# Performance work log

Hardware: AMD Instinct MI355X
Metric: run time of the kernel (lower is better)

## Reference

```python
import jax, jax.numpy as jnp
import numpy as np
from jax import lax

B, N, C = 32, 2048, 256
S, NSAMP, RADIUS = 128, 16, 0.3
NH, NS, NC = 12, 10, 10
OUT_DIM = 5 + 2 * NH + 4 * NS + NC  # 79
EPS = 1e-5
MEAN_SIZES = np.array([[0.76584, 1.398258, 0.472728], [2.114256, 1.6203, 0.927272], [0.404671, 1.071108, 1.688889], [0.591958, 0.552978, 0.827272], [0.69519, 1.346299, 0.736364], [0.528526, 1.002642, 1.172878], [0.500618, 0.632163, 0.683424], [0.923508, 1.867419, 0.845495], [0.791118, 1.279516, 0.718182], [0.699104, 0.454178, 0.75625]], dtype=np.float32)


def _bn(x, g, be, m, v):
    # eval-mode batchnorm over trailing channel dim
    return (x - m) * (g / jnp.sqrt(v + EPS)) + be


def _fps(xyz, npoint):
    # farthest point sampling, sequential over npoint via scan, vectorized over batch
    Bb, Nn, _ = xyz.shape
    def step(carry, _):
        mind, last = carry  # [B,N], [B]
        lp = jnp.take_along_axis(xyz, last[:, None, None], axis=1)  # [B,1,3]
        d = jnp.sum((xyz - lp) ** 2, axis=-1)
        mind = jnp.minimum(mind, d)
        nxt = jnp.argmax(mind, axis=-1).astype(jnp.int32)
        return (mind, nxt), last
    init = (jnp.full((Bb, Nn), 1e10, xyz.dtype), jnp.zeros((Bb,), jnp.int32))
    _, inds = lax.scan(step, init, None, length=npoint)
    return jnp.transpose(inds)  # [B, npoint]


def _ball_query(xyz, new_xyz, radius, nsample):
    # first-nsample points within radius of each center (pad with first hit)
    Nn = xyz.shape[1]
    d2 = jnp.sum((new_xyz[:, :, None, :] - xyz[:, None, :, :]) ** 2, axis=-1)  # [B,S,N]
    cand = jnp.where(d2 < radius * radius, jnp.arange(Nn, dtype=jnp.int32)[None, None, :], Nn)
    idx = jnp.sort(cand, axis=-1)[..., :nsample]
    first = idx[..., :1]  # center itself is always within radius (d=0)
    return jnp.where(idx == Nn, first, idx)


def _forward(xyz, features, w0, bb0, g0, be0, m0, v0, w1, bb1, g1, be1, m1, v1, w2, bb2, g2, be2, m2, v2, c1w, c1b, g3, be3, m3, v3, c2w, c2b, g4, be4, m4, v4, c3w, c3b):
    fps_idx = _fps(xyz, S)  # [B,S]
    new_xyz = jnp.take_along_axis(xyz, fps_idx[..., None], axis=1)  # [B,S,3]
    idx = _ball_query(xyz, new_xyz, RADIUS, NSAMP)  # [B,S,ns]
    bidx = jnp.arange(xyz.shape[0])[:, None, None]
    g_xyz = (xyz[bidx, idx] - new_xyz[:, :, None, :]) / RADIUS  # normalize_xyz
    g_feat = jnp.transpose(features, (0, 2, 1))[bidx, idx]  # [B,S,ns,C]
    x = jnp.concatenate([g_xyz, g_feat], axis=-1)  # [B,S,ns,C+3]
    for w, bb, g, be, m, v in ((w0, bb0, g0, be0, m0, v0), (w1, bb1, g1, be1, m1, v1), (w2, bb2, g2, be2, m2, v2)):
        x = jax.nn.relu(_bn(x @ w + bb, g, be, m, v))
    x = jnp.max(x, axis=2)  # [B,S,128] pooled features
    net = jax.nn.relu(_bn(x @ c1w + c1b, g3, be3, m3, v3))
    net = jax.nn.relu(_bn(net @ c2w + c2b, g4, be4, m4, v4))
    net = net @ c3w + c3b  # [B,S,79] == torch net.transpose(2,1)
    obj = net[..., 0:2]
    ctr = new_xyz + net[..., 2:5]
    hs = net[..., 5:5 + NH]
    hrn = net[..., 5 + NH:5 + 2 * NH]
    hr = hrn * jnp.float32(np.pi / NH)
    ss = net[..., 5 + 2 * NH:5 + 2 * NH + NS]
    srn = net[..., 5 + 2 * NH + NS:5 + 2 * NH + 4 * NS].reshape(net.shape[0], S, NS, 3)
    sr = srn * jnp.asarray(MEAN_SIZES)[None, None]
    sem = net[..., 5 + 2 * NH + 4 * NS:]
    return jnp.concatenate([new_xyz, obj, ctr, hs, hrn, hr, ss, srn.reshape(net.shape[0], S, NS * 3), sr.reshape(net.shape[0], S, NS * 3), sem], axis=-1)  # [B,S,124]


def setup_inputs() -> dict:
    key = jax.random.key(0)
    ks = jax.random.split(key, 40)
    def w(k, shp):
        return jax.random.normal(k, shp, jnp.float32) * 0.05
    d = {"xyz": jax.random.normal(ks[0], (B, N, 3), jnp.float32), "features": jax.random.normal(ks[1], (B, C, N), jnp.float32)}
    i = 2
    for li, (cin, cout) in enumerate(((C + 3, 128), (128, 128), (128, 128))):
        d[f"w{li}"] = w(ks[i], (cin, cout)); d[f"bb{li}"] = w(ks[i + 1], (cout,))
        d[f"g{li}"] = 1.0 + w(ks[i + 2], (cout,)); d[f"be{li}"] = w(ks[i + 3], (cout,))
        d[f"m{li}"] = w(ks[i + 4], (cout,)); d[f"v{li}"] = jnp.ones((cout,), jnp.float32)
        i += 5
    d["c1w"] = w(ks[i], (128, 128)); d["c1b"] = w(ks[i + 1], (128,))
    d["g3"] = 1.0 + w(ks[i + 2], (128,)); d["be3"] = w(ks[i + 3], (128,)); d["m3"] = w(ks[i + 4], (128,)); d["v3"] = jnp.ones((128,), jnp.float32)
    d["c2w"] = w(ks[i + 5], (128, 128)); d["c2b"] = w(ks[i + 6], (128,))
    d["g4"] = 1.0 + w(ks[i + 7], (128,)); d["be4"] = w(ks[i + 8], (128,)); d["m4"] = w(ks[i + 9], (128,)); d["v4"] = jnp.ones((128,), jnp.float32)
    d["c3w"] = w(ks[i + 10], (128, OUT_DIM)); d["c3b"] = w(ks[i + 11], (OUT_DIM,))
    return d


def reference(xyz, features, w0, bb0, g0, be0, m0, v0, w1, bb1, g1, be1, m1, v1, w2, bb2, g2, be2, m2, v2, c1w, c1b, g3, be3, m3, v3, c2w, c2b, g4, be4, m4, v4, c3w, c3b):
    return _forward(xyz, features, w0, bb0, g0, be0, m0, v0, w1, bb1, g1, be1, m1, v1, w2, bb2, g2, be2, m2, v2, c1w, c1b, g3, be3, m3, v3, c2w, c2b, g4, be4, m4, v4, c3w, c3b)
```

## Files before the change

### kernel.cpp

```cpp
#include <hip/hip_runtime.h>
#include <hip/hip_bf16.h>
#include <math.h>

#define Bn 32
#define Nn 2048
#define Cc 256
#define Sn 128
#define KK 16
#define H 128
#define OUTC 79
#define ODIM 124
#define KP1 288

typedef __attribute__((ext_vector_type(8))) short short8;
typedef __attribute__((ext_vector_type(4))) float f32x4;
typedef unsigned long long ull;

__device__ __constant__ float MEANF[30] = {
    0.76584f, 1.398258f, 0.472728f,
    2.114256f, 1.6203f, 0.927272f,
    0.404671f, 1.071108f, 1.688889f,
    0.591958f, 0.552978f, 0.827272f,
    0.69519f, 1.346299f, 0.736364f,
    0.528526f, 1.002642f, 1.172878f,
    0.500618f, 0.632163f, 0.683424f,
    0.923508f, 1.867419f, 0.845495f,
    0.791118f, 1.279516f, 0.718182f,
    0.699104f, 0.454178f, 0.75625f};

__device__ __forceinline__ unsigned short f2bf(float f) {
    __hip_bfloat16 h = __float2bfloat16(f);
    return *reinterpret_cast<unsigned short*>(&h);
}

__device__ __forceinline__ ull umax64(ull a, ull b) { return a > b ? a : b; }

struct SmemFPS {
    float xs[Nn * 3];
    ull red[2][4];
    float nx[Sn * 3];
};
struct SmemT {
    float tile[64][33];
};
__global__ __launch_bounds__(256) void fps_transpose_kernel(const float* __restrict__ xyz,
                                                            const float* __restrict__ features,
                                                            float* __restrict__ new_xyz,
                                                            unsigned short* __restrict__ fT) {
    __shared__ __align__(16) char smem_raw[sizeof(SmemT) > sizeof(SmemFPS) ? sizeof(SmemT)
                                                                           : sizeof(SmemFPS)];
    const int bid = blockIdx.x;
    if (bid >= Bn) {
        SmemT* sm = (SmemT*)smem_raw;
        const int tb = bid - Bn;
        const int b = tb >> 8;
        const int rem = tb & 255;
        const int n0 = (rem & 63) * 32;
        const int c0 = (rem >> 6) * 64;
        const int tx = threadIdx.x & 31;
        const int ty = threadIdx.x >> 5;
        for (int i = ty; i < 64; i += 8)
            sm->tile[i][tx] = features[((size_t)b * Cc + (c0 + i)) * Nn + n0 + tx];
        __syncthreads();
        for (int n = ty; n < 32; n += 8) {
            const float lo = sm->tile[tx * 2 + 0][n];
            const float hi = sm->tile[tx * 2 + 1][n];
            const unsigned int v = (unsigned int)f2bf(lo) | ((unsigned int)f2bf(hi) << 16);
            *reinterpret_cast<unsigned int*>(&fT[((size_t)b * Nn + (n0 + n)) * Cc + c0 + tx * 2]) = v;
        }
        return;
    }
    {
#pragma clang fp contract(off)
        SmemFPS* sm = (SmemFPS*)smem_raw;
        float* xs = sm->xs;
        const int b = bid;
        const int t = threadIdx.x;
        const int lane = t & 63;
        const int wv = t >> 6;

        {
            float4* xs4 = (float4*)xs;
            const float4* src = (const float4*)(xyz + (size_t)b * Nn * 3);
            for (int i = t; i < Nn * 3 / 4; i += 256) xs4[i] = src[i];
        }
        __syncthreads();

        const int base = wv * 512 + lane;
        float px[8], py[8], pz[8], mind[8];
        int klo[8];
#pragma unroll
        for (int j = 0; j < 8; j++) {
            const int p = base + j * 64;
            px[j] = xs[p * 3 + 0];
            py[j] = xs[p * 3 + 1];
            pz[j] = xs[p * 3 + 2];
            mind[j] = 1e10f;
            klo[j] = 2047 - p;
        }
        float lx = xs[0], ly = xs[1], lz = xs[2];

        for (int it = 0; it < Sn; ++it) {
            if (t == 0) {
                sm->nx[it * 3 + 0] = lx;
                sm->nx[it * 3 + 1] = ly;
                sm->nx[it * 3 + 2] = lz;
            }
            ull kk[8];
#pragma unroll
            for (int j = 0; j < 8; j++) {
                const float dx = px[j] - lx;
                const float dy = py[j] - ly;
                const float dz = pz[j] - lz;
                const float dx2 = dx * dx;
                const float dy2 = dy * dy;
                const float dz2 = dz * dz;
                const float s01 = dx2 + dy2;
                const float d = s01 + dz2;
                const float m = fminf(mind[j], d);
                mind[j] = m;
                kk[j] = ((ull)__float_as_uint(m) << 32) | (unsigned int)klo[j];
            }
            ull k0 = umax64(kk[0], kk[1]);
            ull k1 = umax64(kk[2], kk[3]);
            ull k2 = umax64(kk[4], kk[5]);
            ull k3 = umax64(kk[6], kk[7]);
            k0 = umax64(k0, k1);
            k2 = umax64(k2, k3);
            ull bk = umax64(k0, k2);
#pragma unroll
            for (int off = 1; off < 64; off <<= 1) {
                const ull o = __shfl_xor(bk, off);
                bk = umax64(bk, o);
            }
            if (lane == 0) sm->red[it & 1][wv] = bk;
            __syncthreads();
            ull r0 = sm->red[it & 1][0];
            ull r1 = sm->red[it & 1][1];
            ull r2 = sm->red[it & 1][2];
            ull r3 = sm->red[it & 1][3];
            bk = umax64(umax64(r0, r1), umax64(r2, r3));
            const int last = 2047 - (int)(bk & 0xffffffffull);
            lx = xs[last * 3 + 0];
            ly = xs[last * 3 + 1];
            lz = xs[last * 3 + 2];
        }
        __syncthreads();
        for (int i = t; i < Sn * 3; i += 256)
            new_xyz[(size_t)b * Sn * 3 + i] = sm->nx[i];
    }
}

__device__ __forceinline__ float w0val(const float* __restrict__ w0, int n, int k) {
    if (k < 256) return w0[(3 + k) * H + n];
    if (k < 259) return w0[(k - 256) * H + n];
    return 0.0f;
}

__global__ __launch_bounds__(256) void prep_kernel(
    const float* __restrict__ w0, const float* __restrict__ bb0,
    const float* __restrict__ g0, const float* __restrict__ be0,
    const float* __restrict__ m0, const float* __restrict__ v0,
    const float* __restrict__ w1, const float* __restrict__ bb1,
    const float* __restrict__ g1, const float* __restrict__ be1,
    const float* __restrict__ m1, const float* __restrict__ v1,
    const float* __restrict__ w2, const float* __restrict__ bb2,
    const float* __restrict__ g2, const float* __restrict__ be2,
    const float* __restrict__ m2, const float* __restrict__ v2,
    const float* __restrict__ c1w, const float* __restrict__ c1b,
    const float* __restrict__ g3, const float* __restrict__ be3,
    const float* __restrict__ m3, const float* __restrict__ v3,
    const float* __restrict__ c2w, const float* __restrict__ c2b,
    const float* __restrict__ g4, const float* __restrict__ be4,
    const float* __restrict__ m4, const float* __restrict__ v4,
    const float* __restrict__ c3w, const float* __restrict__ c3b,
    unsigned short* __restrict__ Wf0, unsigned short* __restrict__ Wf1,
    unsigned short* __restrict__ Wf2, unsigned short* __restrict__ Wfc1,
    unsigned short* __restrict__ Wfc2, unsigned short* __restrict__ Wfc3,
    float* __restrict__ scbi, float* __restrict__ scbiH) {
    const int idx = blockIdx.x * 256 + threadIdx.x;

    if (idx < 4608) {
        const int kc = idx / 512;
        const int rem = idx & 511;
        const int nt = rem >> 6;
        const int lane = rem & 63;
        const int n = nt * 16 + (lane & 15);
        const int kb = kc * 32 + (lane >> 4) * 8;
        union { unsigned short u[8]; uint4 q; } P;
#pragma unroll
        for (int j = 0; j < 8; j++) P.u[j] = f2bf(w0val(w0, n, kb + j));
        ((uint4*)Wf0)[idx] = P.q;
    }
    if (idx < 2048) {
        const int kc = idx >> 9;
        const int rem = idx & 511;
        const int nt = rem >> 6;
        const int lane = rem & 63;
        const int n = nt * 16 + (lane & 15);
        const int kb = kc * 32 + (lane >> 4) * 8;
        union { unsigned short u[8]; uint4 q; } P1, P2, P3, P4;
#pragma unroll
        for (int j = 0; j < 8; j++) {
            const int k = kb + j;
            P1.u[j] = f2bf(w1[k * H + n]);
            P2.u[j] = f2bf(w2[k * H + n]);
            P3.u[j] = f2bf(c1w[k * H + n]);
            P4.u[j] = f2bf(c2w[k * H + n]);
        }
        ((uint4*)Wf1)[idx] = P1.q;
        ((uint4*)Wf2)[idx] = P2.q;
        ((uint4*)Wfc1)[idx] = P3.q;
        ((uint4*)Wfc2)[idx] = P4.q;
    }
    if (idx < 1280) {
        const int kc = idx / 320;
        const int rem = idx % 320;
        const int nt = rem / 64;
        const int lane = rem % 64;
        const int n = nt * 16 + (lane & 15);
        const int kb = kc * 32 + (lane >> 4) * 8;
        union { unsigned short u[8]; uint4 q; } P;
#pragma unroll
        for (int j = 0; j < 8; j++)
            P.u[j] = (n < OUTC) ? f2bf(c3w[(kb + j) * OUTC + n]) : (unsigned short)0;
        ((uint4*)Wfc3)[idx] = P.q;
    }
    if (idx < 128) {
        const float sc1 = g0[idx] / sqrtf(v0[idx] + 1e-5f);
        scbi[0 * 128 + idx] = sc1;
        scbi[1 * 128 + idx] = (bb0[idx] - m0[idx]) * sc1 + be0[idx];
        const float sc2 = g1[idx] / sqrtf(v1[idx] + 1e-5f);
        scbi[2 * 128 + idx] = sc2;
        scbi[3 * 128 + idx] = (bb1[idx] - m1[idx]) * sc2 + be1[idx];
        const float sc3 = g2[idx] / sqrtf(v2[idx] + 1e-5f);
        scbi[4 * 128 + idx] = sc3;
        scbi[5 * 128 + idx] = (bb2[idx] - m2[idx]) * sc3 + be2[idx];
        const float sA = g3[idx] / sqrtf(v3[idx] + 1e-5f);
        scbiH[0 * 128 + idx] = sA;
        scbiH[1 * 128 + idx] = (c1b[idx] - m3[idx]) * sA + be3[idx];
        const float sB = g4[idx] / sqrtf(v4[idx] + 1e-5f);
        scbiH[2 * 128 + idx] = sB;
        scbiH[3 * 128 + idx] = (c2b[idx] - m4[idx]) * sB + be4[idx];
    }
    if (idx < 80) scbiH[512 + idx] = (idx < OUTC) ? c3b[idx] : 0.0f;
}

#define YSTR 136
__global__ __launch_bounds__(256) void groupmlp_mfma_kernel(
    const float* __restrict__ xyz, const unsigned short* __restrict__ featT,
    const float* __restrict__ new_xyz,
    const unsigned short* __restrict__ Wf0, const unsigned short* __restrict__ Wf1,
    const unsigned short* __restrict__ Wf2, const float* __restrict__ scbi,
    unsigned short* __restrict__ pooledb) {
    const int wv = threadIdx.x >> 6;
    const int lane = threadIdx.x & 63;
    const int bs = blockIdx.x * 4 + wv;
    const int b = bs >> 7;
    const int mrow = lane & 15;
    const int quad = lane >> 4;

    __shared__ unsigned short ylds_all[4][16 * YSTR];
    __shared__ int sbuf[4][16];
    unsigned short* ylds = &ylds_all[wv][0];

    const float cx = new_xyz[bs * 3 + 0];
    const float cy = new_xyz[bs * 3 + 1];
    const float cz = new_xyz[bs * 3 + 2];
    int basec = 0;
    {
#pragma clang fp contract(off)
        for (int c0 = 0; c0 < Nn && basec < KK; c0 += 64) {
            const int p = c0 + lane;
            const float dx = xyz[((size_t)b * Nn + p) * 3 + 0] - cx;
            const float dy = xyz[((size_t)b * Nn + p) * 3 + 1] - cy;
            const float dz = xyz[((size_t)b * Nn + p) * 3 + 2] - cz;
            const float dx2 = dx * dx;
            const float dy2 = dy * dy;
            const float dz2 = dz * dz;
            const float s01 = dx2 + dy2;
            const float d2 = s01 + dz2;
            const bool q = d2 < 0.09f;
            const ull mask = __ballot(q);
            const int prefix = __popcll(mask & ((1ull << lane) - 1ull));
            const int slot = basec + prefix;
            if (q && slot < KK) sbuf[wv][slot] = p;
            basec += __popcll(mask);
        }
    }
    const int cnt = basec < KK ? basec : KK;
    const int p = sbuf[wv][mrow < cnt ? mrow : 0];

    const short8* arow = reinterpret_cast<const short8*>(featT + ((size_t)(b * Nn + p)) * Cc);

    short8 a1x = {0, 0, 0, 0, 0, 0, 0, 0};
    {
        const float fx = xyz[((size_t)(b * Nn + p)) * 3 + 0];
        const float fy = xyz[((size_t)(b * Nn + p)) * 3 + 1];
        const float fz = xyz[((size_t)(b * Nn + p)) * 3 + 2];
        if (quad == 0) {
            a1x.s0 = (short)f2bf((fx - cx) / 0.3f);
            a1x.s1 = (short)f2bf((fy - cy) / 0.3f);
            a1x.s2 = (short)f2bf((fz - cz) / 0.3f);
        }
    }

    const short8* wf0 = reinterpret_cast<const short8*>(Wf0);
    const short8* wf1 = reinterpret_cast<const short8*>(Wf1);
    const short8* wf2 = reinterpret_cast<const short8*>(Wf2);
    const short8* yv = reinterpret_cast<const short8*>(ylds);

    f32x4 acc[8] = {};

    {
        short8 acur = arow[quad];
        short8 anxt;
        short8 bcur[8], bnxt[8];
#pragma unroll
        for (int nt = 0; nt < 8; nt++)
            bcur[nt] = wf0[nt * 64 + lane];
        for (int kc = 0; kc < 9; kc++) {
            if (kc < 8) {
                if (kc < 7) anxt = arow[(kc + 1) * 4 + quad];
                else anxt = a1x;
#pragma unroll
                for (int nt = 0; nt < 8; nt++)
                    bnxt[nt] = wf0[((kc + 1) * 8 + nt) * 64 + lane];
            }
#pragma unroll
            for (int nt = 0; nt < 8; nt++)
                acc[nt] = __builtin_amdgcn_mfma_f32_16x16x32_bf16(acur, bcur[nt], acc[nt], 0, 0, 0);
            acur = anxt;
#pragma unroll
            for (int nt = 0; nt < 8; nt++) bcur[nt] = bnxt[nt];
        }
    }
#pragma unroll
    for (int nt = 0; nt < 8; nt++) {
        const int n = nt * 16 + mrow;
        const float sc = scbi[0 * 128 + n];
        const float bi = scbi[1 * 128 + n];
#pragma unroll
        for (int r = 0; r < 4; r++) {
            const float z = fmaxf(acc[nt][r] * sc + bi, 0.0f);
            ylds[(quad * 4 + r) * YSTR + n] = f2bf(z);
        }
    }

#pragma unroll
    for (int nt = 0; nt < 8; nt++) acc[nt] = (f32x4){0.f, 0.f, 0.f, 0.f};
    {
        short8 acur = yv[mrow * (YSTR / 8) + quad];
        short8 anxt;
        short8 bcur[8], bnxt[8];
#pragma unroll
        for (int nt = 0; nt < 8; nt++)
            bcur[nt] = wf1[nt * 64 + lane];
        for (int kc = 0; kc < 4; kc++) {
            if (kc < 3) {
                anxt = yv[mrow * (YSTR / 8) + (kc + 1) * 4 + quad];
#pragma unroll
                for (int nt = 0; nt < 8; nt++)
                    bnxt[nt] = wf1[((kc + 1) * 8 + nt) * 64 + lane];
            }
#pragma unroll
            for (int nt = 0; nt < 8; nt++)
                acc[nt] = __builtin_amdgcn_mfma_f32_16x16x32_bf16(acur, bcur[nt], acc[nt], 0, 0, 0);
            acur = anxt;
#pragma unroll
            for (int nt = 0; nt < 8; nt++) bcur[nt] = bnxt[nt];
        }
    }
#pragma unroll
    for (int nt = 0; nt < 8; nt++) {
        const int n = nt * 16 + mrow;
        const float sc = scbi[2 * 128 + n];
        const float bi = scbi[3 * 128 + n];
#pragma unroll
        for (int r = 0; r < 4; r++) {
            const float z = fmaxf(acc[nt][r] * sc + bi, 0.0f);
            ylds[(quad * 4 + r) * YSTR + n] = f2bf(z);
        }
    }

#pragma unroll
    for (int nt = 0; nt < 8; nt++) acc[nt] = (f32x4){0.f, 0.f, 0.f, 0.f};
    {
        short8 acur = yv[mrow * (YSTR / 8) + quad];
        short8 anxt;
        short8 bcur[8], bnxt[8];
#pragma unroll
        for (int nt = 0; nt < 8; nt++)
            bcur[nt] = wf2[nt * 64 + lane];
        for (int kc = 0; kc < 4; kc++) {
            if (kc < 3) {
                anxt = yv[mrow * (YSTR / 8) + (kc + 1) * 4 + quad];
#pragma unroll
                for (int nt = 0; nt < 8; nt++)
                    bnxt[nt] = wf2[((kc + 1) * 8 + nt) * 64 + lane];
            }
#pragma unroll
            for (int nt = 0; nt < 8; nt++)
                acc[nt] = __builtin_amdgcn_mfma_f32_16x16x32_bf16(acur, bcur[nt], acc[nt], 0, 0, 0);
            acur = anxt;
#pragma unroll
            for (int nt = 0; nt < 8; nt++) bcur[nt] = bnxt[nt];
        }
    }
#pragma unroll
    for (int nt = 0; nt < 8; nt++) {
        const int n = nt * 16 + mrow;
        const float sc = scbi[4 * 128 + n];
        const float bi = scbi[5 * 128 + n];
        float vmax = 0.0f;
#pragma unroll
        for (int r = 0; r < 4; r++)
            vmax = fmaxf(vmax, acc[nt][r] * sc + bi);
        vmax = fmaxf(vmax, __shfl_xor(vmax, 16));
        vmax = fmaxf(vmax, __shfl_xor(vmax, 32));
        if (quad == 0) pooledb[(size_t)bs * H + n] = f2bf(vmax);
    }
}

__global__ __launch_bounds__(64) void head_mfma_kernel(
    const unsigned short* __restrict__ pooledb, const float* __restrict__ new_xyz,
    const unsigned short* __restrict__ Wfc1, const unsigned short* __restrict__ Wfc2,
    const unsigned short* __restrict__ Wfc3, const float* __restrict__ scbiH,
    float* __restrict__ out) {
    const int lane = threadIdx.x;
    const int row0 = blockIdx.x * 16;
    const int mrow = lane & 15;
    const int quad = lane >> 4;

    __shared__ unsigned short ylds[16 * YSTR];
    __shared__ float flds[16 * 84];

    const short8* ar = reinterpret_cast<const short8*>(pooledb + (size_t)(row0 + mrow) * H);
    const short8* w1h = reinterpret_cast<const short8*>(Wfc1);
    const short8* w2h = reinterpret_cast<const short8*>(Wfc2);
    const short8* w3h = reinterpret_cast<const short8*>(Wfc3);
    const short8* yv = reinterpret_cast<const short8*>(ylds);

    f32x4 acc[8] = {};
#pragma unroll
    for (int kc = 0; kc < 4; kc++) {
        const short8 a = ar[kc * 4 + quad];
#pragma unroll
        for (int nt = 0; nt < 8; nt++) {
            const short8 bf = w1h[(kc * 8 + nt) * 64 + lane];
            acc[nt] = __builtin_amdgcn_mfma_f32_16x16x32_bf16(a, bf, acc[nt], 0, 0, 0);
        }
    }
#pragma unroll
    for (int nt = 0; nt < 8; nt++) {
        const int n = nt * 16 + mrow;
        const float sc = scbiH[0 * 128 + n];
        const float bi = scbiH[1 * 128 + n];
#pragma unroll
        for (int r = 0; r < 4; r++) {
            const float z = fmaxf(acc[nt][r] * sc + bi, 0.0f);
            ylds[(quad * 4 + r) * YSTR + n] = f2bf(z);
        }
    }

#pragma unroll
    for (int nt = 0; nt < 8; nt++) acc[nt] = (f32x4){0.f, 0.f, 0.f, 0.f};
#pragma unroll
    for (int kc = 0; kc < 4; kc++) {
        const short8 a = yv[mrow * (YSTR / 8) + kc * 4 + quad];
#pragma unroll
        for (int nt = 0; nt < 8; nt++) {
            const short8 bf = w2h[(kc * 8 + nt) * 64 + lane];
            acc[nt] = __builtin_amdgcn_mfma_f32_16x16x32_bf16(a, bf, acc[nt], 0, 0, 0);
        }
    }
#pragma unroll
    for (int nt = 0; nt < 8; nt++) {
        const int n = nt * 16 + mrow;
        const float sc = scbiH[2 * 128 + n];
        const float bi = scbiH[3 * 128 + n];
#pragma unroll
        for (int r = 0; r < 4; r++) {
            const float z = fmaxf(acc[nt][r] * sc + bi, 0.0f);
            ylds[(quad * 4 + r) * YSTR + n] = f2bf(z);
        }
    }

    f32x4 acc3[5] = {};
#pragma unroll
    for (int kc = 0; kc < 4; kc++) {
        const short8 a = yv[mrow * (YSTR / 8) + kc * 4 + quad];
#pragma unroll
        for (int nt = 0; nt < 5; nt++) {
            const short8 bf = w3h[(kc * 5 + nt) * 64 + lane];
            acc3[nt] = __builtin_amdgcn_mfma_f32_16x16x32_bf16(a, bf, acc3[nt], 0, 0, 0);
        }
    }
#pragma unroll
    for (int nt = 0; nt < 5; nt++) {
        const int n = nt * 16 + mrow;
        const float bi = scbiH[512 + n];
#pragma unroll
        for (int r = 0; r < 4; r++)
            flds[(quad * 4 + r) * 84 + n] = acc3[nt][r] + bi;
    }

    for (int m = 0; m < 16; m++) {
        const int row = row0 + m;
        const float* net = &flds[m * 84];
        const float* nz = new_xyz + (size_t)row * 3;
#pragma unroll
        for (int jj = 0; jj < 2; jj++) {
            const int j = lane + jj * 64;
            if (j < ODIM) {
                float val;
                if (j < 3) val = nz[j];
                else if (j < 5) val = net[j - 3];
                else if (j < 8) val = nz[j - 5] + net[2 + (j - 5)];
                else if (j < 20) val = net[5 + (j - 8)];
                else if (j < 32) val = net[17 + (j - 20)];
                else if (j < 44) val = net[17 + (j - 32)] * (float)(3.14159265358979323846 / 12.0);
                else if (j < 54) val = net[29 + (j - 44)];
                else if (j < 84) val = net[39 + (j - 54)];
                else if (j < 114) val = net[39 + (j - 84)] * MEANF[j - 84];
                else val = net[69 + (j - 114)];
                out[(size_t)row * ODIM + j] = val;
            }
        }
    }
}

extern "C" void kernel_launch(void* const* d_in, const int* in_sizes, int n_in,
                              void* d_out, int out_size, void* d_ws, size_t ws_size,
                              hipStream_t stream) {
    (void)in_sizes; (void)n_in; (void)out_size; (void)ws_size;
    const float* xyz = (const float*)d_in[0];
    const float* features = (const float*)d_in[1];
    const float* w0 = (const float*)d_in[2];
    const float* bb0 = (const float*)d_in[3];
    const float* g0 = (const float*)d_in[4];
    const float* be0 = (const float*)d_in[5];
    const float* m0 = (const float*)d_in[6];
    const float* v0 = (const float*)d_in[7];
    const float* w1 = (const float*)d_in[8];
    const float* bb1 = (const float*)d_in[9];
    const float* g1 = (const float*)d_in[10];
    const float* be1 = (const float*)d_in[11];
    const float* m1 = (const float*)d_in[12];
    const float* v1 = (const float*)d_in[13];
    const float* w2 = (const float*)d_in[14];
    const float* bb2 = (const float*)d_in[15];
    const float* g2 = (const float*)d_in[16];
    const float* be2 = (const float*)d_in[17];
    const float* m2 = (const float*)d_in[18];
    const float* v2 = (const float*)d_in[19];
    const float* c1w = (const float*)d_in[20];
    const float* c1b = (const float*)d_in[21];
    const float* g3 = (const float*)d_in[22];
    const float* be3 = (const float*)d_in[23];
    const float* m3 = (const float*)d_in[24];
    const float* v3 = (const float*)d_in[25];
    const float* c2w = (const float*)d_in[26];
    const float* c2b = (const float*)d_in[27];
    const float* g4 = (const float*)d_in[28];
    const float* be4 = (const float*)d_in[29];
    const float* m4 = (const float*)d_in[30];
    const float* v4 = (const float*)d_in[31];
    const float* c3w = (const float*)d_in[32];
    const float* c3b = (const float*)d_in[33];
    float* out = (float*)d_out;

    char* ws = (char*)d_ws;
    float* nxyz = (float*)(ws + 0);
    float* scbi = (float*)(ws + 49152);
    float* scbiH = (float*)(ws + 52224);
    unsigned short* Wf0 = (unsigned short*)(ws + 54592);
    unsigned short* Wf1 = (unsigned short*)(ws + 128320);
    unsigned short* Wf2 = (unsigned short*)(ws + 161088);
    unsigned short* Wfc1 = (unsigned short*)(ws + 193856);
    unsigned short* Wfc2 = (unsigned short*)(ws + 226624);
    unsigned short* Wfc3 = (unsigned short*)(ws + 259392);
    unsigned short* pooledb = (unsigned short*)(ws + 279872);
    unsigned short* featT = (unsigned short*)(ws + 804160);

    hipLaunchKernelGGL(prep_kernel, dim3(18), dim3(256), 0, stream,
                       w0, bb0, g0, be0, m0, v0,
                       w1, bb1, g1, be1, m1, v1,
                       w2, bb2, g2, be2, m2, v2,
                       c1w, c1b, g3, be3, m3, v3,
                       c2w, c2b, g4, be4, m4, v4,
                       c3w, c3b,
                       Wf0, Wf1, Wf2, Wfc1, Wfc2, Wfc3, scbi, scbiH);
    hipLaunchKernelGGL(fps_transpose_kernel, dim3(Bn + Bn * 256), dim3(256), 0, stream,
                       xyz, features, nxyz, featT);
    hipLaunchKernelGGL(groupmlp_mfma_kernel, dim3(Bn * Sn / 4), dim3(256), 0, stream,
                       xyz, featT, nxyz, Wf0, Wf1, Wf2, scbi, pooledb);
    hipLaunchKernelGGL(head_mfma_kernel, dim3(Bn * Sn / 16), dim3(64), 0, stream,
                       pooledb, nxyz, Wfc1, Wfc2, Wfc3, scbiH, out);
}
```

Baseline: 302.8 us.

## Fuse prep into FPS/transpose kernel and carry coordinates through FPS argmax reduction

Merges the weight-prep kernel into the FPS/transpose launch as extra blocks, which removes one kernel launch. The FPS loop now carries the winning point's coordinates through the argmax reduction, so each iteration no longer has to look up the chosen point in a shared xyz copy. That shared copy is removed, which shrinks LDS use. The cross-lane reduction uses ds_swizzle and a final bpermute in place of 64-bit shfl_xor; each step moves five 32-bit values instead of one 64-bit key.

```diff
diff --git a/kernel.cpp b/kernel.cpp
--- a/kernel.cpp
+++ b/kernel.cpp
@@ -33,131 +33,34 @@
     return *reinterpret_cast<unsigned short*>(&h);
 }
 
-__device__ __forceinline__ ull umax64(ull a, ull b) { return a > b ? a : b; }
+__device__ __forceinline__ float w0val(const float* __restrict__ w0, int n, int k) {
+    if (k < 256) return w0[(3 + k) * H + n];
+    if (k < 259) return w0[(k - 256) * H + n];
+    return 0.0f;
+}
+
+#define BFLY_SWZ(PAT)                                                          \
+    {                                                                          \
+        const int ohi = __builtin_amdgcn_ds_swizzle(hi, PAT);                  \
+        const int olo = __builtin_amdgcn_ds_swizzle(lo, PAT);                  \
+        const int oxi = __builtin_amdgcn_ds_swizzle(xi, PAT);                  \
+        const int oyi = __builtin_amdgcn_ds_swizzle(yi, PAT);                  \
+        const int ozi = __builtin_amdgcn_ds_swizzle(zi, PAT);                  \
+        const ull ok = ((ull)(unsigned)ohi << 32) | (unsigned)olo;             \
+        const ull ck = ((ull)(unsigned)hi << 32) | (unsigned)lo;               \
+        if (ok > ck) { hi = ohi; lo = olo; xi = oxi; yi = oyi; zi = ozi; }     \
+    }
 
 struct SmemFPS {
-    float xs[Nn * 3];
-    ull red[2][4];
+    int red[2][4][8];
     float nx[Sn * 3];
 };
 struct SmemT {
     float tile[64][33];
 };
-__global__ __launch_bounds__(256) void fps_transpose_kernel(const float* __restrict__ xyz,
-                                                            const float* __restrict__ features,
-                                                            float* __restrict__ new_xyz,
-                                                            unsigned short* __restrict__ fT) {
-    __shared__ __align__(16) char smem_raw[sizeof(SmemT) > sizeof(SmemFPS) ? sizeof(SmemT)
-                                                                           : sizeof(SmemFPS)];
-    const int bid = blockIdx.x;
-    if (bid >= Bn) {
-        SmemT* sm = (SmemT*)smem_raw;
-        const int tb = bid - Bn;
-        const int b = tb >> 8;
-        const int rem = tb & 255;
-        const int n0 = (rem & 63) * 32;
-        const int c0 = (rem >> 6) * 64;
-        const int tx = threadIdx.x & 31;
-        const int ty = threadIdx.x >> 5;
-        for (int i = ty; i < 64; i += 8)
-            sm->tile[i][tx] = features[((size_t)b * Cc + (c0 + i)) * Nn + n0 + tx];
-        __syncthreads();
-        for (int n = ty; n < 32; n += 8) {
-            const float lo = sm->tile[tx * 2 + 0][n];
-            const float hi = sm->tile[tx * 2 + 1][n];
-            const unsigned int v = (unsigned int)f2bf(lo) | ((unsigned int)f2bf(hi) << 16);
-            *reinterpret_cast<unsigned int*>(&fT[((size_t)b * Nn + (n0 + n)) * Cc + c0 + tx * 2]) = v;
-        }
-        return;
-    }
-    {
-#pragma clang fp contract(off)
-        SmemFPS* sm = (SmemFPS*)smem_raw;
-        float* xs = sm->xs;
-        const int b = bid;
-        const int t = threadIdx.x;
-        const int lane = t & 63;
-        const int wv = t >> 6;
-
-        {
-            float4* xs4 = (float4*)xs;
-            const float4* src = (const float4*)(xyz + (size_t)b * Nn * 3);
-            for (int i = t; i < Nn * 3 / 4; i += 256) xs4[i] = src[i];
-        }
-        __syncthreads();
-
-        const int base = wv * 512 + lane;
-        float px[8], py[8], pz[8], mind[8];
-        int klo[8];
-#pragma unroll
-        for (int j = 0; j < 8; j++) {
-            const int p = base + j * 64;
-            px[j] = xs[p * 3 + 0];
-            py[j] = xs[p * 3 + 1];
-            pz[j] = xs[p * 3 + 2];
-            mind[j] = 1e10f;
-            klo[j] = 2047 - p;
-        }
-        float lx = xs[0], ly = xs[1], lz = xs[2];
-
-        for (int it = 0; it < Sn; ++it) {
-            if (t == 0) {
-                sm->nx[it * 3 + 0] = lx;
-                sm->nx[it * 3 + 1] = ly;
-                sm->nx[it * 3 + 2] = lz;
-            }
-            ull kk[8];
-#pragma unroll
-            for (int j = 0; j < 8; j++) {
-                const float dx = px[j] - lx;
-                const float dy = py[j] - ly;
-                const float dz = pz[j] - lz;
-                const float dx2 = dx * dx;
-                const float dy2 = dy * dy;
-                const float dz2 = dz * dz;
-                const float s01 = dx2 + dy2;
-                const float d = s01 + dz2;
-                const float m = fminf(mind[j], d);
-                mind[j] = m;
-                kk[j] = ((ull)__float_as_uint(m) << 32) | (unsigned int)klo[j];
-            }
-            ull k0 = umax64(kk[0], kk[1]);
-            ull k1 = umax64(kk[2], kk[3]);
-            ull k2 = umax64(kk[4], kk[5]);
-            ull k3 = umax64(kk[6], kk[7]);
-            k0 = umax64(k0, k1);
-            k2 = umax64(k2, k3);
-            ull bk = umax64(k0, k2);
-#pragma unroll
-            for (int off = 1; off < 64; off <<= 1) {
-                const ull o = __shfl_xor(bk, off);
-                bk = umax64(bk, o);
-            }
-            if (lane == 0) sm->red[it & 1][wv] = bk;
-            __syncthreads();
-            ull r0 = sm->red[it & 1][0];
-            ull r1 = sm->red[it & 1][1];
-            ull r2 = sm->red[it & 1][2];
-            ull r3 = sm->red[it & 1][3];
-            bk = umax64(umax64(r0, r1), umax64(r2, r3));
-            const int last = 2047 - (int)(bk & 0xffffffffull);
-            lx = xs[last * 3 + 0];
-            ly = xs[last * 3 + 1];
-            lz = xs[last * 3 + 2];
-        }
-        __syncthreads();
-        for (int i = t; i < Sn * 3; i += 256)
-            new_xyz[(size_t)b * Sn * 3 + i] = sm->nx[i];
-    }
-}
-
-__device__ __forceinline__ float w0val(const float* __restrict__ w0, int n, int k) {
-    if (k < 256) return w0[(3 + k) * H + n];
-    if (k < 259) return w0[(k - 256) * H + n];
-    return 0.0f;
-}
-
-__global__ __launch_bounds__(256) void prep_kernel(
+__global__ __launch_bounds__(256) void fused_front_kernel(
+    const float* __restrict__ xyz, const float* __restrict__ features,
+    float* __restrict__ new_xyz, unsigned short* __restrict__ fT,
     const float* __restrict__ w0, const float* __restrict__ bb0,
     const float* __restrict__ g0, const float* __restrict__ be0,
     const float* __restrict__ m0, const float* __restrict__ v0,
@@ -178,72 +81,196 @@
     unsigned short* __restrict__ Wf2, unsigned short* __restrict__ Wfc1,
     unsigned short* __restrict__ Wfc2, unsigned short* __restrict__ Wfc3,
     float* __restrict__ scbi, float* __restrict__ scbiH) {
-    const int idx = blockIdx.x * 256 + threadIdx.x;
-
-    if (idx < 4608) {
-        const int kc = idx / 512;
-        const int rem = idx & 511;
-        const int nt = rem >> 6;
-        const int lane = rem & 63;
-        const int n = nt * 16 + (lane & 15);
-        const int kb = kc * 32 + (lane >> 4) * 8;
-        union { unsigned short u[8]; uint4 q; } P;
-#pragma unroll
-        for (int j = 0; j < 8; j++) P.u[j] = f2bf(w0val(w0, n, kb + j));
-        ((uint4*)Wf0)[idx] = P.q;
-    }
-    if (idx < 2048) {
-        const int kc = idx >> 9;
-        const int rem = idx & 511;
-        const int nt = rem >> 6;
-        const int lane = rem & 63;
-        const int n = nt * 16 + (lane & 15);
-        const int kb = kc * 32 + (lane >> 4) * 8;
-        union { unsigned short u[8]; uint4 q; } P1, P2, P3, P4;
+    __shared__ __align__(16) char smem_raw[sizeof(SmemT) > sizeof(SmemFPS) ? sizeof(SmemT)
+                                                                           : sizeof(SmemFPS)];
+    const int bid = blockIdx.x;
+    if (bid >= Bn + 8192) {
+        const int idx = (bid - (Bn + 8192)) * 256 + threadIdx.x;
+        if (idx < 4608) {
+            const int kc = idx / 512;
+            const int rem = idx & 511;
+            const int nt = rem >> 6;
+            const int lane = rem & 63;
+            const int n = nt * 16 + (lane & 15);
+            const int kb = kc * 32 + (lane >> 4) * 8;
+            union { unsigned short u[8]; uint4 q; } P;
+#pragma unroll
+            for (int j = 0; j < 8; j++) P.u[j] = f2bf(w0val(w0, n, kb + j));
+            ((uint4*)Wf0)[idx] = P.q;
+        }
+        if (idx < 2048) {
+            const int kc = idx >> 9;
+            const int rem = idx & 511;
+            const int nt = rem >> 6;
+            const int lane = rem & 63;
+            const int n = nt * 16 + (lane & 15);
+            const int kb = kc * 32 + (lane >> 4) * 8;
+            union { unsigned short u[8]; uint4 q; } P1, P2, P3, P4;
+#pragma unroll
+            for (int j = 0; j < 8; j++) {
+                const int k = kb + j;
+                P1.u[j] = f2bf(w1[k * H + n]);
+                P2.u[j] = f2bf(w2[k * H + n]);
+                P3.u[j] = f2bf(c1w[k * H + n]);
+                P4.u[j] = f2bf(c2w[k * H + n]);
+            }
+            ((uint4*)Wf1)[idx] = P1.q;
+            ((uint4*)Wf2)[idx] = P2.q;
+            ((uint4*)Wfc1)[idx] = P3.q;
+            ((uint4*)Wfc2)[idx] = P4.q;
+        }
+        if (idx < 1280) {
+            const int kc = idx / 320;
+            const int rem = idx % 320;
+            const int nt = rem / 64;
+            const int lane = rem % 64;
+            const int n = nt * 16 + (lane & 15);
+            const int kb = kc * 32 + (lane >> 4) * 8;
+            union { unsigned short u[8]; uint4 q; } P;
+#pragma unroll
+            for (int j = 0; j < 8; j++)
+                P.u[j] = (n < OUTC) ? f2bf(c3w[(kb + j) * OUTC + n]) : (unsigned short)0;
+            ((uint4*)Wfc3)[idx] = P.q;
+        }
+        if (idx < 128) {
+            const float sc1 = g0[idx] / sqrtf(v0[idx] + 1e-5f);
+            scbi[0 * 128 + idx] = sc1;
+            scbi[1 * 128 + idx] = (bb0[idx] - m0[idx]) * sc1 + be0[idx];
+            const float sc2 = g1[idx] / sqrtf(v1[idx] + 1e-5f);
+            scbi[2 * 128 + idx] = sc2;
+            scbi[3 * 128 + idx] = (bb1[idx] - m1[idx]) * sc2 + be1[idx];
+            const float sc3 = g2[idx] / sqrtf(v2[idx] + 1e-5f);
+            scbi[4 * 128 + idx] = sc3;
+            scbi[5 * 128 + idx] = (bb2[idx] - m2[idx]) * sc3 + be2[idx];
+            const float sA = g3[idx] / sqrtf(v3[idx] + 1e-5f);
+            scbiH[0 * 128 + idx] = sA;
+            scbiH[1 * 128 + idx] = (c1b[idx] - m3[idx]) * sA + be3[idx];
+            const float sB = g4[idx] / sqrtf(v4[idx] + 1e-5f);
+            scbiH[2 * 128 + idx] = sB;
+            scbiH[3 * 128 + idx] = (c2b[idx] - m4[idx]) * sB + be4[idx];
+        }
+        if (idx < 80) scbiH[512 + idx] = (idx < OUTC) ? c3b[idx] : 0.0f;
+        return;
+    }
+    if (bid >= Bn) {
+        SmemT* sm = (SmemT*)smem_raw;
+        const int tb = bid - Bn;
+        const int b = tb >> 8;
+        const int rem = tb & 255;
+        const int n0 = (rem & 63) * 32;
+        const int c0 = (rem >> 6) * 64;
+        const int tx = threadIdx.x & 31;
+        const int ty = threadIdx.x >> 5;
+        for (int i = ty; i < 64; i += 8)
+            sm->tile[i][tx] = features[((size_t)b * Cc + (c0 + i)) * Nn + n0 + tx];
+        __syncthreads();
+        for (int n = ty; n < 32; n += 8) {
+            const float lo2 = sm->tile[tx * 2 + 0][n];
+            const float hi2 = sm->tile[tx * 2 + 1][n];
+            const unsigned int v = (unsigned int)f2bf(lo2) | ((unsigned int)f2bf(hi2) << 16);
+            *reinterpret_cast<unsigned int*>(&fT[((size_t)b * Nn + (n0 + n)) * Cc + c0 + tx * 2]) = v;
+        }
+        return;
+    }
+    {
+#pragma clang fp contract(off)
+        SmemFPS* sm = (SmemFPS*)smem_raw;
+        const int b = bid;
+        const int t = threadIdx.x;
+        const int lane = t & 63;
+        const int wv = t >> 6;
+        const int p32addr = ((lane ^ 32) << 2);
+
+        const float* xb = xyz + (size_t)b * Nn * 3;
+        float px[8], py[8], pz[8], mind[8];
+        int klo[8];
 #pragma unroll
         for (int j = 0; j < 8; j++) {
-            const int k = kb + j;
-            P1.u[j] = f2bf(w1[k * H + n]);
-            P2.u[j] = f2bf(w2[k * H + n]);
-            P3.u[j] = f2bf(c1w[k * H + n]);
-            P4.u[j] = f2bf(c2w[k * H + n]);
-        }
-        ((uint4*)Wf1)[idx] = P1.q;
-        ((uint4*)Wf2)[idx] = P2.q;
-        ((uint4*)Wfc1)[idx] = P3.q;
-        ((uint4*)Wfc2)[idx] = P4.q;
-    }
-    if (idx < 1280) {
-        const int kc = idx / 320;
-        const int rem = idx % 320;
-        const int nt = rem / 64;
-        const int lane = rem % 64;
-        const int n = nt * 16 + (lane & 15);
-        const int kb = kc * 32 + (lane >> 4) * 8;
-        union { unsigned short u[8]; uint4 q; } P;
-#pragma unroll
-        for (int j = 0; j < 8; j++)
-            P.u[j] = (n < OUTC) ? f2bf(c3w[(kb + j) * OUTC + n]) : (unsigned short)0;
-        ((uint4*)Wfc3)[idx] = P.q;
-    }
-    if (idx < 128) {
-        const float sc1 = g0[idx] / sqrtf(v0[idx] + 1e-5f);
-        scbi[0 * 128 + idx] = sc1;
-        scbi[1 * 128 + idx] = (bb0[idx] - m0[idx]) * sc1 + be0[idx];
-        const float sc2 = g1[idx] / sqrtf(v1[idx] + 1e-5f);
-        scbi[2 * 128 + idx] = sc2;
-        scbi[3 * 128 + idx] = (bb1[idx] - m1[idx]) * sc2 + be1[idx];
-        const float sc3 = g2[idx] / sqrtf(v2[idx] + 1e-5f);
-        scbi[4 * 128 + idx] = sc3;
-        scbi[5 * 128 + idx] = (bb2[idx] - m2[idx]) * sc3 + be2[idx];
-        const float sA = g3[idx] / sqrtf(v3[idx] + 1e-5f);
-        scbiH[0 * 128 + idx] = sA;
-        scbiH[1 * 128 + idx] = (c1b[idx] - m3[idx]) * sA + be3[idx];
-        const float sB = g4[idx] / sqrtf(v4[idx] + 1e-5f);
-        scbiH[2 * 128 + idx] = sB;
-        scbiH[3 * 128 + idx] = (c2b[idx] - m4[idx]) * sB + be4[idx];
-    }
-    if (idx < 80) scbiH[512 + idx] = (idx < OUTC) ? c3b[idx] : 0.0f;
+            const int p = wv * 512 + lane + j * 64;
+            px[j] = xb[p * 3 + 0];
+            py[j] = xb[p * 3 + 1];
+            pz[j] = xb[p * 3 + 2];
+            mind[j] = 1e10f;
+            klo[j] = 2047 - p;
+        }
+        float lx = xb[0], ly = xb[1], lz = xb[2];
+
+        for (int it = 0; it < Sn; ++it) {
+            if (t == 0) {
+                sm->nx[it * 3 + 0] = lx;
+                sm->nx[it * 3 + 1] = ly;
+                sm->nx[it * 3 + 2] = lz;
+            }
+            ull bkey = 0;
+            float bx = 0.f, by = 0.f, bz = 0.f;
+#pragma unroll
+            for (int j = 0; j < 8; j++) {
+                const float dx = px[j] - lx;
+                const float dy = py[j] - ly;
+                const float dz = pz[j] - lz;
+                const float dx2 = dx * dx;
+                const float dy2 = dy * dy;
+                const float dz2 = dz * dz;
+                const float s01 = dx2 + dy2;
+                const float d = s01 + dz2;
+                const float m = fminf(mind[j], d);
+                mind[j] = m;
+                const ull k = ((ull)__float_as_uint(m) << 32) | (unsigned int)klo[j];
+                if (k > bkey) { bkey = k; bx = px[j]; by = py[j]; bz = pz[j]; }
+            }
+            int hi = (int)(bkey >> 32);
+            int lo = (int)(bkey & 0xffffffffull);
+            int xi = __float_as_int(bx);
+            int yi = __float_as_int(by);
+            int zi = __float_as_int(bz);
+            BFLY_SWZ(0x041F)
+            BFLY_SWZ(0x081F)
+            BFLY_SWZ(0x101F)
+            BFLY_SWZ(0x201F)
+            BFLY_SWZ(0x401F)
+            {
+                const int ohi = __builtin_amdgcn_ds_bpermute(p32addr, hi);
+                const int olo = __builtin_amdgcn_ds_bpermute(p32addr, lo);
+                const int oxi = __builtin_amdgcn_ds_bpermute(p32addr, xi);
+                const int oyi = __builtin_amdgcn_ds_bpermute(p32addr, yi);
+                const int ozi = __builtin_amdgcn_ds_bpermute(p32addr, zi);
+                const ull ok = ((ull)(unsigned)ohi << 32) | (unsigned)olo;
+                const ull ck = ((ull)(unsigned)hi << 32) | (unsigned)lo;
+                if (ok > ck) { hi = ohi; lo = olo; xi = oxi; yi = oyi; zi = ozi; }
+            }
+            const int par = it & 1;
+            if (lane == 0) {
+                int* slot = &sm->red[par][wv][0];
+                ((int4*)slot)[0] = make_int4(hi, lo, xi, yi);
+                slot[4] = zi;
+            }
+            __syncthreads();
+            {
+                const int4 s0 = ((const int4*)&sm->red[par][0][0])[0];
+                const int4 s1 = ((const int4*)&sm->red[par][1][0])[0];
+                const int4 s2 = ((const int4*)&sm->red[par][2][0])[0];
+                const int4 s3 = ((const int4*)&sm->red[par][3][0])[0];
+                const int z0 = sm->red[par][0][4];
+                const int z1 = sm->red[par][1][4];
+                const int z2 = sm->red[par][2][4];
+                const int z3 = sm->red[par][3][4];
+                ull bk = ((ull)(unsigned)s0.x << 32) | (unsigned)s0.y;
+                int wxi = s0.z, wyi = s0.w, wzi = z0;
+                ull ok = ((ull)(unsigned)s1.x << 32) | (unsigned)s1.y;
+                if (ok > bk) { bk = ok; wxi = s1.z; wyi = s1.w; wzi = z1; }
+                ok = ((ull)(unsigned)s2.x << 32) | (unsigned)s2.y;
+                if (ok > bk) { bk = ok; wxi = s2.z; wyi = s2.w; wzi = z2; }
+                ok = ((ull)(unsigned)s3.x << 32) | (unsigned)s3.y;
+                if (ok > bk) { bk = ok; wxi = s3.z; wyi = s3.w; wzi = z3; }
+                lx = __int_as_float(wxi);
+                ly = __int_as_float(wyi);
+                lz = __int_as_float(wzi);
+            }
+        }
+        __syncthreads();
+        for (int i = t; i < Sn * 3; i += 256)
+            new_xyz[(size_t)b * Sn * 3 + i] = sm->nx[i];
+    }
 }
 
 #define YSTR 136
@@ -583,7 +610,8 @@
     unsigned short* pooledb = (unsigned short*)(ws + 279872);
     unsigned short* featT = (unsigned short*)(ws + 804160);
 
-    hipLaunchKernelGGL(prep_kernel, dim3(18), dim3(256), 0, stream,
+    hipLaunchKernelGGL(fused_front_kernel, dim3(Bn + 8192 + 18), dim3(256), 0, stream,
+                       xyz, features, nxyz, featT,
                        w0, bb0, g0, be0, m0, v0,
                        w1, bb1, g1, be1, m1, v1,
                        w2, bb2, g2, be2, m2, v2,
@@ -591,8 +619,6 @@
                        c2w, c2b, g4, be4, m4, v4,
                        c3w, c3b,
                        Wf0, Wf1, Wf2, Wfc1, Wfc2, Wfc3, scbi, scbiH);
-    hipLaunchKernelGGL(fps_transpose_kernel, dim3(Bn + Bn * 256), dim3(256), 0, stream,
-                       xyz, features, nxyz, featT);
     hipLaunchKernelGGL(groupmlp_mfma_kernel, dim3(Bn * Sn / 4), dim3(256), 0, stream,
                        xyz, featT, nxyz, Wf0, Wf1, Wf2, scbi, pooledb);
     hipLaunchKernelGGL(head_mfma_kernel, dim3(Bn * Sn / 16), dim3(64), 0, stream,
```

New measurement: 324.2 us. 7.1% more time.
